# Kernel optimization log

Hardware: AMD Instinct MI355X
Metric: run time of the kernel (lower is better)

The kernel has to match this reference:

```python
import jax, jax.numpy as jnp
import numpy as np

BATCH, T, H = 2048, 32, 1024
IN_DIM = 2  # [prev_pred, fd_step]

def setup_inputs() -> dict:
    key = jax.random.key(0)
    ks = jax.random.split(key, 9)
    s_ih = 1.0 / np.sqrt(H)
    return {
        "future_fd": jax.random.normal(ks[0], (BATCH, T), jnp.float32),
        "hidden": jax.random.normal(ks[1], (1, BATCH, H), jnp.float32),
        "cell": jax.random.normal(ks[2], (1, BATCH, H), jnp.float32),
        "W_ih": jax.random.uniform(ks[3], (4 * H, IN_DIM), jnp.float32, -s_ih, s_ih),
        "W_hh": jax.random.uniform(ks[4], (4 * H, H), jnp.float32, -s_ih, s_ih),
        "b_ih": jax.random.uniform(ks[5], (4 * H,), jnp.float32, -s_ih, s_ih),
        "b_hh": jax.random.uniform(ks[6], (4 * H,), jnp.float32, -s_ih, s_ih),
        "fc_W": jax.random.uniform(ks[7], (1, H), jnp.float32, -s_ih, s_ih),
        "fc_b": jax.random.uniform(ks[8], (1,), jnp.float32, -s_ih, s_ih),
        "output_len": T,
    }

def reference(future_fd, hidden, cell, W_ih, W_hh, b_ih, b_hh, fc_W, fc_b, output_len):
    # Inference path (targets=None): decoder input is previous prediction.
    h0, c0 = hidden[0], cell[0]            # (B, H), num_layers == 1
    b = b_ih + b_hh                        # (4H,)
    prev0 = jnp.zeros((future_fd.shape[0], 1), future_fd.dtype)

    def step(carry, fd_t):
        h, c, prev = carry
        x = jnp.concatenate([prev, fd_t[:, None]], axis=1)   # (B, 2)
        gates = x @ W_ih.T + h @ W_hh.T + b                  # (B, 4H)
        i, f, g, o = jnp.split(gates, 4, axis=1)             # PyTorch gate order i,f,g,o
        c_new = jax.nn.sigmoid(f) * c + jax.nn.sigmoid(i) * jnp.tanh(g)
        h_new = jax.nn.sigmoid(o) * jnp.tanh(c_new)
        pred = h_new @ fc_W.T + fc_b                          # (B, 1)
        return (h_new, c_new, pred), pred

    _, preds = jax.lax.scan(step, (h0, c0, prev0), future_fd.T)  # (T, B, 1)
    return jnp.transpose(preds, (1, 0, 2))                       # (B, T, 1)
```

## Files before the change

### kernel.cpp

```cpp
#include <hip/hip_runtime.h>
#include <hip/hip_bf16.h>

#define TSTEPS 32
#define HDIM 1024

typedef __bf16 bf16x8 __attribute__((ext_vector_type(8)));
typedef float f32x4 __attribute__((ext_vector_type(4)));
typedef unsigned short u16;
typedef unsigned int u32;

__device__ __forceinline__ u32 f2bf(float f) {
    u32 u = __float_as_uint(f);
    return (u + 0x7FFFu + ((u >> 16) & 1u)) >> 16;
}
__device__ __forceinline__ u32 pack2(float a, float b) {
    return f2bf(a) | (f2bf(b) << 16);
}
__device__ __forceinline__ float sigf(float x) { return 1.f / (1.f + __expf(-x)); }
__device__ __forceinline__ float tanhfast(float x) { return 1.f - 2.f / (1.f + __expf(2.f * x)); }


__global__ void k_prep_w(const float* __restrict__ W, const float* __restrict__ Wih,
                         const float* __restrict__ fcW, uint4* __restrict__ Wp) {
    int o = blockIdx.x * 256 + threadIdx.x;
    int colT = o >> 14, c = (o >> 10) & 15, l = o & 1023;
    int bc = l >> 3, u = l & 7;
    int jg = ((bc >> 5) << 10) + colT * 32 + (bc & 31);
    int kk = c * 64 + ((u ^ (bc & 7)) << 3);
    const float4* src  = (const float4*)(W + (size_t)jg * HDIM + kk);
    const float4* fsrc = (const float4*)(fcW + kk);
    float wx = Wih[2 * jg];
    float4 lo = src[0], hi = src[1], fl = fsrc[0], fh = fsrc[1];
    lo.x += wx * fl.x; lo.y += wx * fl.y; lo.z += wx * fl.z; lo.w += wx * fl.w;
    hi.x += wx * fh.x; hi.y += wx * fh.y; hi.z += wx * fh.z; hi.w += wx * fh.w;
    uint4 pk = { pack2(lo.x, lo.y), pack2(lo.z, lo.w), pack2(hi.x, hi.y), pack2(hi.z, hi.w) };
    Wp[o] = pk;
}

__global__ void k_prep_state(const float* __restrict__ h0, const float* __restrict__ c0,
                             u16* __restrict__ hb, float* __restrict__ c) {
    int i = blockIdx.x * 256 + threadIdx.x;
    float4 v = ((const float4*)h0)[i];
    ushort4 o = { (u16)f2bf(v.x), (u16)f2bf(v.y), (u16)f2bf(v.z), (u16)f2bf(v.w) };
    ((ushort4*)hb)[i] = o;
    ((float4*)c)[i] = ((const float4*)c0)[i];
}

__global__ void k_prep_p0(const float* __restrict__ h0, const float* __restrict__ fcW,
                          const float* __restrict__ fcb, float* __restrict__ p0) {
    int n = blockIdx.x * 4 + (threadIdx.x >> 6);
    int lane = threadIdx.x & 63;
    const float* hr = h0 + (size_t)n * HDIM;
    float s = 0.f;
#pragma unroll
    for (int i = 0; i < 16; ++i)
        s += fcW[lane + 64 * i] * hr[lane + 64 * i];
    s += __shfl_xor(s, 1);  s += __shfl_xor(s, 2);  s += __shfl_xor(s, 4);
    s += __shfl_xor(s, 8);  s += __shfl_xor(s, 16); s += __shfl_xor(s, 32);
    if (lane == 0) p0[n] = s + fcb[0];
}

__global__ void k_init_out(float* __restrict__ out, const float* __restrict__ fcb) {
    int i = blockIdx.x * 256 + threadIdx.x;
    out[i] = fcb[0];
}

__device__ __forceinline__ void stage_chunk(const uint4* __restrict__ g, uint4* dst, int tid) {
    const uint4* g0 = g + tid;
    uint4* l0 = dst + (tid & ~63);
#pragma unroll
    for (int i = 0; i < 4; ++i)
        __builtin_amdgcn_global_load_lds(
            (const __attribute__((address_space(1))) void*)(g0 + i * 512),
            (__attribute__((address_space(3))) void*)(l0 + i * 512), 16, 0, 0);
}

__global__ __launch_bounds__(512, 4) void k_step(
    const u16* __restrict__ hin, u16* __restrict__ hout,
    float* __restrict__ c, const uint4* __restrict__ Wp,
    const float* __restrict__ fd, const float* __restrict__ Wih,
    const float* __restrict__ bih, const float* __restrict__ bhh,
    const float* __restrict__ fcw, const float* __restrict__ fcb,
    const float* __restrict__ p0, float* out, int t)
{
    __shared__ uint4 lbuf[2][2048];
    __shared__ float pp[2][128];

    const int tid  = threadIdx.x;
    const int lane = tid & 63;
    const int wave = tid >> 6;
    const int lr = lane & 15, lk = lane >> 4;
    const int wc = wave & 1, wr = wave >> 1;
    const int colT = blockIdx.x;
    const int rowT = blockIdx.y;
    const uint4* wbase = Wp + colT * 16384;

    const u16* arow = hin + (size_t)(rowT * 128 + wr * 32 + lr) * HDIM + lk * 8;

    f32x4 acc[2][4];
#pragma unroll
    for (int a = 0; a < 2; ++a)
#pragma unroll
        for (int g = 0; g < 4; ++g)
            acc[a][g] = (f32x4){0.f, 0.f, 0.f, 0.f};

    bf16x8 A0[2][4], A1[2][4];
#pragma unroll
    for (int kcl = 0; kcl < 4; ++kcl) {
        A0[0][kcl] = *(const bf16x8*)(arow + kcl * 32);
        A1[0][kcl] = *(const bf16x8*)(arow + 16 * HDIM + kcl * 32);
    }
    stage_chunk(wbase, &lbuf[0][0], tid);
    __syncthreads();

#pragma unroll
    for (int ch = 0; ch < 8; ++ch) {
        if (ch < 7) {
            stage_chunk(wbase + (ch + 1) * 2048, &lbuf[(ch + 1) & 1][0], tid);
#pragma unroll
            for (int kcl = 0; kcl < 4; ++kcl) {
                const int kg = (ch + 1) * 4 + kcl;
                A0[(ch + 1) & 1][kcl] = *(const bf16x8*)(arow + kg * 32);
                A1[(ch + 1) & 1][kcl] = *(const bf16x8*)(arow + 16 * HDIM + kg * 32);
            }
        }
        const uint4* buf = &lbuf[ch & 1][0];
#pragma unroll
        for (int kcl = 0; kcl < 4; ++kcl) {
            bf16x8 a0 = A0[ch & 1][kcl];
            bf16x8 a1 = A1[ch & 1][kcl];
#pragma unroll
            for (int cf = 0; cf < 4; ++cf) {
                const int bc = cf * 32 + wc * 16 + lr;
                uint4 braw = buf[(kcl >> 1) * 1024 + bc * 8 +
                                 ((((kcl & 1) << 2) + lk) ^ (bc & 7))];
                bf16x8 bfr = __builtin_bit_cast(bf16x8, braw);
                acc[0][cf] = __builtin_amdgcn_mfma_f32_16x16x32_bf16(a0, bfr, acc[0][cf], 0, 0, 0);
                acc[1][cf] = __builtin_amdgcn_mfma_f32_16x16x32_bf16(a1, bfr, acc[1][cf], 0, 0, 0);
            }
        }
        __syncthreads();
    }

    const int j = colT * 32 + wc * 16 + lr;
    float wx0[4], wx1[4], bs[4];
#pragma unroll
    for (int g = 0; g < 4; ++g) {
        int gr = g * HDIM + j;
        wx0[g] = Wih[2 * gr];
        wx1[g] = Wih[2 * gr + 1];
        bs[g]  = bih[gr] + bhh[gr];
    }
    const float fcwj = fcw[j];
    const float fcbv = fcb[0];

#pragma unroll
    for (int ar = 0; ar < 2; ++ar)
#pragma unroll
        for (int r = 0; r < 4; ++r) {
            const int n = rowT * 128 + wr * 32 + ar * 16 + lk * 4 + r;
            float fdv  = fd[n * TSTEPS + t];
            float pc   = (t == 0) ? (fcbv - p0[n]) : fcbv;
            float gi = acc[ar][0][r] + wx1[0] * fdv + bs[0] + wx0[0] * pc;
            float gf = acc[ar][1][r] + wx1[1] * fdv + bs[1] + wx0[1] * pc;
            float gg = acc[ar][2][r] + wx1[2] * fdv + bs[2] + wx0[2] * pc;
            float go = acc[ar][3][r] + wx1[3] * fdv + bs[3] + wx0[3] * pc;
            float cold = c[(size_t)n * HDIM + j];
            float cn = sigf(gf) * cold + sigf(gi) * tanhfast(gg);
            c[(size_t)n * HDIM + j] = cn;
            float hn = sigf(go) * tanhfast(cn);
            hout[(size_t)n * HDIM + j] = (u16)f2bf(hn);
            float pr = fcwj * hn;
            pr += __shfl_xor(pr, 1);
            pr += __shfl_xor(pr, 2);
            pr += __shfl_xor(pr, 4);
            pr += __shfl_xor(pr, 8);
            if (lr == 0) pp[wc][wr * 32 + ar * 16 + lk * 4 + r] = pr;
        }
    __syncthreads();
    if (tid < 128) {
        int n = rowT * 128 + tid;
        atomicAdd(&out[n * TSTEPS + t], pp[0][tid] + pp[1][tid]);
    }
}

extern "C" void kernel_launch(void* const* d_in, const int* in_sizes, int n_in,
                              void* d_out, int out_size, void* d_ws, size_t ws_size,
                              hipStream_t stream) {
    const float* fd  = (const float*)d_in[0];
    const float* h0  = (const float*)d_in[1];
    const float* c0  = (const float*)d_in[2];
    const float* Wih = (const float*)d_in[3];
    const float* Whh = (const float*)d_in[4];
    const float* bih = (const float*)d_in[5];
    const float* bhh = (const float*)d_in[6];
    const float* fcw = (const float*)d_in[7];
    const float* fcb = (const float*)d_in[8];
    float* out = (float*)d_out;

    char* ws = (char*)d_ws;
    uint4* Wp   = (uint4*)(ws);
    u16*   hb0  = (u16*)(ws + 8388608);
    u16*   hb1  = (u16*)(ws + 12582912);
    float* cbuf = (float*)(ws + 16777216);
    float* p0   = (float*)(ws + 25165824);

    k_prep_w    <<<dim3(2048), dim3(256), 0, stream>>>(Whh, Wih, fcw, Wp);
    k_prep_state<<<dim3(2048), dim3(256), 0, stream>>>(h0, c0, hb0, cbuf);
    k_prep_p0   <<<dim3(512),  dim3(256), 0, stream>>>(h0, fcw, fcb, p0);
    k_init_out  <<<dim3(256),  dim3(256), 0, stream>>>(out, fcb);

    for (int t = 0; t < TSTEPS; ++t) {
        const u16* hi = (t & 1) ? hb1 : hb0;
        u16*       ho = (t & 1) ? hb0 : hb1;
        k_step<<<dim3(32, 16), dim3(512), 0, stream>>>(hi, ho, cbuf, Wp, fd,
                                                        Wih, bih, bhh, fcw, fcb,
                                                        p0, out, t);
    }
}
```

Measured before the change: 1.409 ms.

## Use 32x32 MFMA with fragment-packed h and W, drop LDS staging, bf16 cell

Weights and hidden state are stored pre-swizzled in MFMA fragment order, so each lane loads its A and B operands straight from global memory and the LDS double-buffering and barriers go away. The kernel switches to 32x32x16 MFMA with 256-thread blocks and maps blocks so that each XCD gets a compact tile region, which should help L2 reuse. The cell state is now stored as bf16 to halve its traffic, and each wave issues its per-row prediction atomics directly instead of reducing through shared memory first. Storing the cell in bf16 loses precision across the 32 recurrent steps, and reading B directly from global memory relies on L2 hits for the weight reuse.

```diff
diff --git a/kernel.cpp b/kernel.cpp
--- a/kernel.cpp
+++ b/kernel.cpp
@@ -5,7 +5,7 @@
 #define HDIM 1024
 
 typedef __bf16 bf16x8 __attribute__((ext_vector_type(8)));
-typedef float f32x4 __attribute__((ext_vector_type(4)));
+typedef float f32x16 __attribute__((ext_vector_type(16)));
 typedef unsigned short u16;
 typedef unsigned int u32;
 
@@ -16,19 +16,29 @@
 __device__ __forceinline__ u32 pack2(float a, float b) {
     return f2bf(a) | (f2bf(b) << 16);
 }
+__device__ __forceinline__ float bf2f(u16 v) {
+    return __uint_as_float(((u32)v) << 16);
+}
 __device__ __forceinline__ float sigf(float x) { return 1.f / (1.f + __expf(-x)); }
 __device__ __forceinline__ float tanhfast(float x) { return 1.f - 2.f / (1.f + __expf(2.f * x)); }
+
+__device__ __forceinline__ f32x16 zero16() {
+    f32x16 v;
+#pragma unroll
+    for (int i = 0; i < 16; ++i) v[i] = 0.f;
+    return v;
+}
 
 
 __global__ void k_prep_w(const float* __restrict__ W, const float* __restrict__ Wih,
                          const float* __restrict__ fcW, uint4* __restrict__ Wp) {
     int o = blockIdx.x * 256 + threadIdx.x;
-    int colT = o >> 14, c = (o >> 10) & 15, l = o & 1023;
-    int bc = l >> 3, u = l & 7;
-    int jg = ((bc >> 5) << 10) + colT * 32 + (bc & 31);
-    int kk = c * 64 + ((u ^ (bc & 7)) << 3);
-    const float4* src  = (const float4*)(W + (size_t)jg * HDIM + kk);
-    const float4* fsrc = (const float4*)(fcW + kk);
+    int colT = o >> 14, u = o & 16383;
+    int s = u >> 8, cf = (u >> 6) & 3, l = u & 63;
+    int jg = cf * 1024 + colT * 32 + (l & 31);
+    int kb = s * 16 + ((l >> 5) << 3);
+    const float4* src  = (const float4*)(W + (size_t)jg * HDIM + kb);
+    const float4* fsrc = (const float4*)(fcW + kb);
     float wx = Wih[2 * jg];
     float4 lo = src[0], hi = src[1], fl = fsrc[0], fh = fsrc[1];
     lo.x += wx * fl.x; lo.y += wx * fl.y; lo.z += wx * fl.z; lo.w += wx * fl.w;
@@ -38,12 +48,18 @@
 }
 
 __global__ void k_prep_state(const float* __restrict__ h0, const float* __restrict__ c0,
-                             u16* __restrict__ hb, float* __restrict__ c) {
-    int i = blockIdx.x * 256 + threadIdx.x;
-    float4 v = ((const float4*)h0)[i];
-    ushort4 o = { (u16)f2bf(v.x), (u16)f2bf(v.y), (u16)f2bf(v.z), (u16)f2bf(v.w) };
-    ((ushort4*)hb)[i] = o;
-    ((float4*)c)[i] = ((const float4*)c0)[i];
+                             u16* __restrict__ hF, u16* __restrict__ cb) {
+    int o = blockIdx.x * 256 + threadIdx.x;
+    int n = o >> 7, j = (o & 127) << 3;
+    const float* hp = h0 + (size_t)n * HDIM + j;
+    float4 lo = *(const float4*)hp, hi = *(const float4*)(hp + 4);
+    uint4 pk = { pack2(lo.x, lo.y), pack2(lo.z, lo.w), pack2(hi.x, hi.y), pack2(hi.z, hi.w) };
+    int unit = ((n >> 5) << 12) + ((j >> 4) << 6) + (n & 31) + (((j >> 3) & 1) << 5);
+    ((uint4*)hF)[unit] = pk;
+    const float* cp = c0 + (size_t)n * HDIM + j;
+    float4 cl = *(const float4*)cp, ch = *(const float4*)(cp + 4);
+    uint4 pc = { pack2(cl.x, cl.y), pack2(cl.z, cl.w), pack2(ch.x, ch.y), pack2(ch.z, ch.w) };
+    *(uint4*)(cb + (size_t)n * HDIM + j) = pc;
 }
 
 __global__ void k_prep_p0(const float* __restrict__ h0, const float* __restrict__ fcW,
@@ -65,84 +81,44 @@
     out[i] = fcb[0];
 }
 
-__device__ __forceinline__ void stage_chunk(const uint4* __restrict__ g, uint4* dst, int tid) {
-    const uint4* g0 = g + tid;
-    uint4* l0 = dst + (tid & ~63);
-#pragma unroll
-    for (int i = 0; i < 4; ++i)
-        __builtin_amdgcn_global_load_lds(
-            (const __attribute__((address_space(1))) void*)(g0 + i * 512),
-            (__attribute__((address_space(3))) void*)(l0 + i * 512), 16, 0, 0);
-}
-
-__global__ __launch_bounds__(512, 4) void k_step(
-    const u16* __restrict__ hin, u16* __restrict__ hout,
-    float* __restrict__ c, const uint4* __restrict__ Wp,
+__global__ __launch_bounds__(256, 2) void k_step(
+    const u16* __restrict__ hinF, u16* __restrict__ houtF,
+    u16* __restrict__ c, const uint4* __restrict__ Wp,
     const float* __restrict__ fd, const float* __restrict__ Wih,
     const float* __restrict__ bih, const float* __restrict__ bhh,
     const float* __restrict__ fcw, const float* __restrict__ fcb,
     const float* __restrict__ p0, float* out, int t)
 {
-    __shared__ uint4 lbuf[2][2048];
-    __shared__ float pp[2][128];
-
     const int tid  = threadIdx.x;
     const int lane = tid & 63;
     const int wave = tid >> 6;
-    const int lr = lane & 15, lk = lane >> 4;
-    const int wc = wave & 1, wr = wave >> 1;
-    const int colT = blockIdx.x;
-    const int rowT = blockIdx.y;
-    const uint4* wbase = Wp + colT * 16384;
+    const int id   = blockIdx.x;
+    const int xcd  = id & 7, k = id >> 3;
+    const int colT = ((xcd & 3) << 3) + (k & 7);
+    const int rowT = ((xcd >> 2) << 3) + (k >> 3);
+    const int nb   = rowT * 128 + wave * 32;
+    const int rg   = rowT * 4 + wave;
 
-    const u16* arow = hin + (size_t)(rowT * 128 + wr * 32 + lr) * HDIM + lk * 8;
+    const uint4* bptr = Wp + (size_t)colT * 16384 + lane;
+    const uint4* aptr = (const uint4*)hinF + (size_t)rg * 4096 + lane;
 
-    f32x4 acc[2][4];
-#pragma unroll
-    for (int a = 0; a < 2; ++a)
-#pragma unroll
-        for (int g = 0; g < 4; ++g)
-            acc[a][g] = (f32x4){0.f, 0.f, 0.f, 0.f};
+    f32x16 acc0 = zero16(), acc1 = zero16(), acc2 = zero16(), acc3 = zero16();
 
-    bf16x8 A0[2][4], A1[2][4];
-#pragma unroll
-    for (int kcl = 0; kcl < 4; ++kcl) {
-        A0[0][kcl] = *(const bf16x8*)(arow + kcl * 32);
-        A1[0][kcl] = *(const bf16x8*)(arow + 16 * HDIM + kcl * 32);
-    }
-    stage_chunk(wbase, &lbuf[0][0], tid);
-    __syncthreads();
-
-#pragma unroll
-    for (int ch = 0; ch < 8; ++ch) {
-        if (ch < 7) {
-            stage_chunk(wbase + (ch + 1) * 2048, &lbuf[(ch + 1) & 1][0], tid);
-#pragma unroll
-            for (int kcl = 0; kcl < 4; ++kcl) {
-                const int kg = (ch + 1) * 4 + kcl;
-                A0[(ch + 1) & 1][kcl] = *(const bf16x8*)(arow + kg * 32);
-                A1[(ch + 1) & 1][kcl] = *(const bf16x8*)(arow + 16 * HDIM + kg * 32);
-            }
-        }
-        const uint4* buf = &lbuf[ch & 1][0];
-#pragma unroll
-        for (int kcl = 0; kcl < 4; ++kcl) {
-            bf16x8 a0 = A0[ch & 1][kcl];
-            bf16x8 a1 = A1[ch & 1][kcl];
-#pragma unroll
-            for (int cf = 0; cf < 4; ++cf) {
-                const int bc = cf * 32 + wc * 16 + lr;
-                uint4 braw = buf[(kcl >> 1) * 1024 + bc * 8 +
-                                 ((((kcl & 1) << 2) + lk) ^ (bc & 7))];
-                bf16x8 bfr = __builtin_bit_cast(bf16x8, braw);
-                acc[0][cf] = __builtin_amdgcn_mfma_f32_16x16x32_bf16(a0, bfr, acc[0][cf], 0, 0, 0);
-                acc[1][cf] = __builtin_amdgcn_mfma_f32_16x16x32_bf16(a1, bfr, acc[1][cf], 0, 0, 0);
-            }
-        }
-        __syncthreads();
+#pragma unroll 4
+    for (int s = 0; s < 64; ++s) {
+        bf16x8 av = __builtin_bit_cast(bf16x8, aptr[s * 64]);
+        bf16x8 b0 = __builtin_bit_cast(bf16x8, bptr[s * 256 + 0]);
+        bf16x8 b1 = __builtin_bit_cast(bf16x8, bptr[s * 256 + 64]);
+        bf16x8 b2 = __builtin_bit_cast(bf16x8, bptr[s * 256 + 128]);
+        bf16x8 b3 = __builtin_bit_cast(bf16x8, bptr[s * 256 + 192]);
+        acc0 = __builtin_amdgcn_mfma_f32_32x32x16_bf16(av, b0, acc0, 0, 0, 0);
+        acc1 = __builtin_amdgcn_mfma_f32_32x32x16_bf16(av, b1, acc1, 0, 0, 0);
+        acc2 = __builtin_amdgcn_mfma_f32_32x32x16_bf16(av, b2, acc2, 0, 0, 0);
+        acc3 = __builtin_amdgcn_mfma_f32_32x32x16_bf16(av, b3, acc3, 0, 0, 0);
     }
 
-    const int j = colT * 32 + wc * 16 + lr;
+    const int jl = lane & 31;
+    const int j  = colT * 32 + jl;
     float wx0[4], wx1[4], bs[4];
 #pragma unroll
     for (int g = 0; g < 4; ++g) {
@@ -153,34 +129,31 @@
     }
     const float fcwj = fcw[j];
     const float fcbv = fcb[0];
+    const int   hjpart = ((j >> 4) << 6) + (((j >> 3) & 1) << 5);
+    const int   je = j & 7;
 
 #pragma unroll
-    for (int ar = 0; ar < 2; ++ar)
-#pragma unroll
-        for (int r = 0; r < 4; ++r) {
-            const int n = rowT * 128 + wr * 32 + ar * 16 + lk * 4 + r;
-            float fdv  = fd[n * TSTEPS + t];
-            float pc   = (t == 0) ? (fcbv - p0[n]) : fcbv;
-            float gi = acc[ar][0][r] + wx1[0] * fdv + bs[0] + wx0[0] * pc;
-            float gf = acc[ar][1][r] + wx1[1] * fdv + bs[1] + wx0[1] * pc;
-            float gg = acc[ar][2][r] + wx1[2] * fdv + bs[2] + wx0[2] * pc;
-            float go = acc[ar][3][r] + wx1[3] * fdv + bs[3] + wx0[3] * pc;
-            float cold = c[(size_t)n * HDIM + j];
-            float cn = sigf(gf) * cold + sigf(gi) * tanhfast(gg);
-            c[(size_t)n * HDIM + j] = cn;
-            float hn = sigf(go) * tanhfast(cn);
-            hout[(size_t)n * HDIM + j] = (u16)f2bf(hn);
-            float pr = fcwj * hn;
-            pr += __shfl_xor(pr, 1);
-            pr += __shfl_xor(pr, 2);
-            pr += __shfl_xor(pr, 4);
-            pr += __shfl_xor(pr, 8);
-            if (lr == 0) pp[wc][wr * 32 + ar * 16 + lk * 4 + r] = pr;
-        }
-    __syncthreads();
-    if (tid < 128) {
-        int n = rowT * 128 + tid;
-        atomicAdd(&out[n * TSTEPS + t], pp[0][tid] + pp[1][tid]);
+    for (int r = 0; r < 16; ++r) {
+        const int n = nb + (r & 3) + ((r >> 2) << 3) + ((lane >> 5) << 2);
+        float fdv = fd[n * TSTEPS + t];
+        float pc  = (t == 0) ? (fcbv - p0[n]) : fcbv;
+        float gi = acc0[r] + wx1[0] * fdv + bs[0] + wx0[0] * pc;
+        float gf = acc1[r] + wx1[1] * fdv + bs[1] + wx0[1] * pc;
+        float gg = acc2[r] + wx1[2] * fdv + bs[2] + wx0[2] * pc;
+        float go = acc3[r] + wx1[3] * fdv + bs[3] + wx0[3] * pc;
+        float cold = bf2f(c[(size_t)n * HDIM + j]);
+        float cn = sigf(gf) * cold + sigf(gi) * tanhfast(gg);
+        c[(size_t)n * HDIM + j] = (u16)f2bf(cn);
+        float hn = sigf(go) * tanhfast(cn);
+        int unit = ((n >> 5) << 12) + hjpart + (n & 31);
+        houtF[unit * 8 + je] = (u16)f2bf(hn);
+        float pr = fcwj * hn;
+        pr += __shfl_xor(pr, 1);
+        pr += __shfl_xor(pr, 2);
+        pr += __shfl_xor(pr, 4);
+        pr += __shfl_xor(pr, 8);
+        pr += __shfl_xor(pr, 16);
+        if (jl == 0) atomicAdd(&out[n * TSTEPS + t], pr);
     }
 }
 
@@ -200,21 +173,21 @@
 
     char* ws = (char*)d_ws;
     uint4* Wp   = (uint4*)(ws);
-    u16*   hb0  = (u16*)(ws + 8388608);
-    u16*   hb1  = (u16*)(ws + 12582912);
-    float* cbuf = (float*)(ws + 16777216);
+    u16*   hF0  = (u16*)(ws + 8388608);
+    u16*   hF1  = (u16*)(ws + 12582912);
+    u16*   cbuf = (u16*)(ws + 16777216);
     float* p0   = (float*)(ws + 25165824);
 
     k_prep_w    <<<dim3(2048), dim3(256), 0, stream>>>(Whh, Wih, fcw, Wp);
-    k_prep_state<<<dim3(2048), dim3(256), 0, stream>>>(h0, c0, hb0, cbuf);
+    k_prep_state<<<dim3(1024), dim3(256), 0, stream>>>(h0, c0, hF0, cbuf);
     k_prep_p0   <<<dim3(512),  dim3(256), 0, stream>>>(h0, fcw, fcb, p0);
     k_init_out  <<<dim3(256),  dim3(256), 0, stream>>>(out, fcb);
 
     for (int t = 0; t < TSTEPS; ++t) {
-        const u16* hi = (t & 1) ? hb1 : hb0;
-        u16*       ho = (t & 1) ? hb0 : hb1;
-        k_step<<<dim3(32, 16), dim3(512), 0, stream>>>(hi, ho, cbuf, Wp, fd,
-                                                        Wih, bih, bhh, fcw, fcb,
-                                                        p0, out, t);
+        const u16* hi = (t & 1) ? hF1 : hF0;
+        u16*       ho = (t & 1) ? hF0 : hF1;
+        k_step<<<dim3(512), dim3(256), 0, stream>>>(hi, ho, cbuf, Wp, fd,
+                                                     Wih, bih, bhh, fcw, fcb,
+                                                     p0, out, t);
     }
 }
```

After: 1.439 ms. 1.02x slower.
